# Kernel optimization log

Measured on AMD Instinct MI355X. Metric: run time of the kernel, lower is better.

Reference implementation:

```python
import jax, jax.numpy as jnp
import numpy as np
from jax import lax

T, H, I, E, K = 1024, 1024, 512, 16, 4


def setup_inputs() -> dict:
    key = jax.random.key(0)
    k1, k2, k3, k4, k5 = jax.random.split(key, 5)
    hidden_states = jax.random.normal(k1, (T, H), dtype=jnp.float32)
    top_k_index = jax.random.randint(k2, (T, K), 0, E)
    top_k_weights = jax.random.uniform(k3, (T, K), dtype=jnp.float32)
    gate_up_proj = jax.random.normal(k4, (E, 2 * I, H), dtype=jnp.float32) * 0.02
    down_proj = jax.random.normal(k5, (E, H, I), dtype=jnp.float32) * 0.02
    return {
        "hidden_states": hidden_states,
        "top_k_index": top_k_index,
        "top_k_weights": top_k_weights,
        "gate_up_proj": gate_up_proj,
        "down_proj": down_proj,
    }


def reference(hidden_states, top_k_index, top_k_weights, gate_up_proj, down_proj):
    num_experts = gate_up_proj.shape[0]
    # combine[t, e] = sum_k top_k_weights[t, k] * [top_k_index[t, k] == e]
    # Expert output is linear in the routing weight, so summing weights over
    # duplicate (token, expert) hits matches the original index_add_ exactly.
    one_hot = jax.nn.one_hot(top_k_index, num_experts, dtype=hidden_states.dtype)  # [T, K, E]
    combine = jnp.einsum("tke,tk->te", one_hot, top_k_weights)  # [T, E]

    def expert_step(acc, xs):
        w_gu, w_d, c = xs  # [2I, H], [H, I], [T]
        gu = hidden_states @ w_gu.T          # [T, 2I]
        gate, up = jnp.split(gu, 2, axis=-1)
        h = jax.nn.silu(gate) * up            # [T, I]
        out = h @ w_d.T                       # [T, H]
        return acc + out * c[:, None], None

    final, _ = lax.scan(
        expert_step,
        jnp.zeros_like(hidden_states),
        (gate_up_proj, down_proj, combine.T),
    )
    return final
```

## Files before the change

kernel.cpp:

```cpp
#include <hip/hip_runtime.h>
#include <hip/hip_bf16.h>
#include <cstdint>
#include <cstddef>

#define T_TOK 1024
#define HDIM  1024
#define IDIM  512
#define NEXP  16
#define TOPK  4
#define CAP   1024
#define GROUP 5

typedef __bf16 bf16;
typedef __attribute__((ext_vector_type(8))) __bf16 bf16x8;
typedef __attribute__((ext_vector_type(4))) __bf16 bf16x4;
typedef __attribute__((ext_vector_type(4))) float f32x4;

__device__ __forceinline__ void lds_load16(void* lds_dst, const void* g_src) {
  __builtin_amdgcn_global_load_lds(
      (__attribute__((address_space(1))) unsigned int*)(void*)(g_src),
      (__attribute__((address_space(3))) unsigned int*)(lds_dst),
      16, 0, 0);
}

__device__ __forceinline__ bf16x4 cvt4(float4 a) {
  bf16x4 o;
  o[0] = (bf16)a.x; o[1] = (bf16)a.y; o[2] = (bf16)a.z; o[3] = (bf16)a.w;
  return o;
}
__device__ __forceinline__ bf16x8 pack2(float4 a, float4 b) {
  bf16x8 o;
  o[0] = (bf16)a.x; o[1] = (bf16)a.y; o[2] = (bf16)a.z; o[3] = (bf16)a.w;
  o[4] = (bf16)b.x; o[5] = (bf16)b.y; o[6] = (bf16)b.z; o[7] = (bf16)b.w;
  return o;
}


#define CVT_BLOCKS (T_TOK * HDIM / 4 / 256)

__global__ void prep_kernel(const float* __restrict__ hid_f, bf16* __restrict__ hid_b,
                            const int* __restrict__ idx, const float* __restrict__ w,
                            int* __restrict__ etk, float* __restrict__ ew,
                            int* __restrict__ cntpad) {
  __shared__ int cnt;
  const int b = blockIdx.x;
  const int tid = threadIdx.x;
  if (b < CVT_BLOCKS) {
    int i = b * 256 + tid;
    float4 v = ((const float4*)hid_f)[i];
    ((bf16x4*)hid_b)[i] = cvt4(v);
    if (b == 0)
      ((bf16x4*)(hid_b + (size_t)T_TOK * HDIM))[tid] = cvt4(make_float4(0.f, 0.f, 0.f, 0.f));
    return;
  }
  const int e = b - CVT_BLOCKS;
  if (tid == 0) cnt = 0;
  __syncthreads();
  for (int j = tid; j < T_TOK * TOPK; j += blockDim.x) {
    if (idx[j] == e) {
      int slot = atomicAdd(&cnt, 1);
      if (slot < CAP) { etk[e * CAP + slot] = j; ew[e * CAP + slot] = w[j]; }
    }
  }
  __syncthreads();
  int c = cnt < CAP ? cnt : CAP;
  int p = (c + 63) & ~63;
  for (int j = c + tid; j < p; j += blockDim.x) {
    etk[e * CAP + j] = (T_TOK << 2);
    ew[e * CAP + j] = 0.f;
  }
  if (tid == 0) cntpad[e] = p;
}


__global__ __launch_bounds__(256, 2) void gemm1_kernel(
    const bf16* __restrict__ hid,
    const float* __restrict__ gup,
    const int* __restrict__ etk, const float* __restrict__ ew,
    const int* __restrict__ cntpad,
    bf16* __restrict__ hsc) {
  __shared__ __align__(16) bf16 As[GROUP][64 * 64];
  __shared__ __align__(16) bf16 BgS[16 * 64];
  __shared__ __align__(16) bf16 BuS[16 * 64];
  const int e  = blockIdx.y;
  const int trips = cntpad[e] >> 6;
  const int n0 = blockIdx.x * 16;
  const int ebase = e * CAP;
  const int tid = threadIdx.x, lane = tid & 63, wid = tid >> 6;
  const int wm = wid * 16;
  const int lcol = lane & 15, lquad = lane >> 4;
  const int srow = tid >> 3;
  const int swz  = ((tid & 7) ^ (srow & 7)) * 8;
  const int br = tid >> 4;
  const int bc = (tid & 15) * 4;
  const int wb = (((bc >> 3) ^ (br & 7)) * 8) + (bc & 7);
  const float* gBg = gup + (size_t)e * (2 * IDIM) * HDIM + (size_t)(n0 + br) * HDIM + bc;
  const float* gBu = gBg + (size_t)IDIM * HDIM;

  for (int mg = 0; mg < trips; mg += GROUP) {
    const int tg = trips - mg < GROUP ? trips - mg : GROUP;
    const bf16 *gA0[GROUP], *gA1[GROUP];
#pragma unroll
    for (int mt = 0; mt < GROUP; ++mt)
      if (mt < tg) {
        const int mb = ebase + (mg + mt) * 64;
        gA0[mt] = hid + (size_t)(etk[mb + srow] >> 2) * HDIM + swz;
        gA1[mt] = hid + (size_t)(etk[mb + srow + 32] >> 2) * HDIM + swz;
      }
    f32x4 aG[GROUP], aU[GROUP];
#pragma unroll
    for (int mt = 0; mt < GROUP; ++mt) {
      aG[mt] = f32x4{0.f, 0.f, 0.f, 0.f};
      aU[mt] = f32x4{0.f, 0.f, 0.f, 0.f};
    }
    for (int k = 0; k < HDIM / 64; ++k) {
      float4 vg = *(const float4*)(gBg + k * 64);
      float4 vu = *(const float4*)(gBu + k * 64);
      __syncthreads();
#pragma unroll
      for (int mt = 0; mt < GROUP; ++mt)
        if (mt < tg) {
          lds_load16(&As[mt][tid * 8],        gA0[mt] + k * 64);
          lds_load16(&As[mt][tid * 8 + 2048], gA1[mt] + k * 64);
        }
      *(bf16x4*)&BgS[br * 64 + wb] = cvt4(vg);
      *(bf16x4*)&BuS[br * 64 + wb] = cvt4(vu);
      __syncthreads();
#pragma unroll
      for (int ks = 0; ks < 2; ++ks) {
        const int lch = ks * 4 + lquad;
        bf16x8 bg = *(const bf16x8*)&BgS[lcol * 64 + ((lch ^ (lcol & 7)) * 8)];
        bf16x8 bu = *(const bf16x8*)&BuS[lcol * 64 + ((lch ^ (lcol & 7)) * 8)];
        const int ar = wm + lcol;
        const int aoff = ar * 64 + ((lch ^ (ar & 7)) * 8);
#pragma unroll
        for (int mt = 0; mt < GROUP; ++mt)
          if (mt < tg) {
            bf16x8 af = *(const bf16x8*)&As[mt][aoff];
            aG[mt] = __builtin_amdgcn_mfma_f32_16x16x32_bf16(af, bg, aG[mt], 0, 0, 0);
            aU[mt] = __builtin_amdgcn_mfma_f32_16x16x32_bf16(af, bu, aU[mt], 0, 0, 0);
          }
      }
    }
#pragma unroll
    for (int mt = 0; mt < GROUP; ++mt)
      if (mt < tg) {
#pragma unroll
        for (int rr = 0; rr < 4; ++rr) {
          const int erow = (mg + mt) * 64 + wm + lquad * 4 + rr;
          const float wgt = ew[ebase + erow];
          float g = aG[mt][rr], u = aU[mt][rr];
          float s = g / (1.f + __expf(-g));
          hsc[(size_t)(ebase + erow) * IDIM + n0 + lcol] = (bf16)(s * u * wgt);
        }
      }
  }
}


__global__ __launch_bounds__(256, 2) void gemm2_kernel(
    const bf16* __restrict__ hsc,
    const float* __restrict__ down,
    const int* __restrict__ etk, const int* __restrict__ cntpad,
    float* __restrict__ slabs) {
  __shared__ __align__(16) bf16 As[GROUP][64 * 64];
  __shared__ __align__(16) bf16 Bs[32 * 64];
  const int e  = blockIdx.y;
  const int trips = cntpad[e] >> 6;
  const int n0 = blockIdx.x * 32;
  const int ebase = e * CAP;
  const int tid = threadIdx.x, lane = tid & 63, wid = tid >> 6;
  const int wm = wid * 16;
  const int lcol = lane & 15, lquad = lane >> 4;
  const int srow = tid >> 3;
  const int swz  = ((tid & 7) ^ (srow & 7)) * 8;
  const int btr = tid >> 3;
  const int c0  = (tid & 7) * 8;
  const int wbk = ((tid & 7) ^ (btr & 7)) * 8;
  const float* gB = down + (size_t)e * HDIM * IDIM + (size_t)(n0 + btr) * IDIM + c0;

  for (int mg = 0; mg < trips; mg += GROUP) {
    const int tg = trips - mg < GROUP ? trips - mg : GROUP;
    f32x4 acc[GROUP][2];
#pragma unroll
    for (int mt = 0; mt < GROUP; ++mt) {
      acc[mt][0] = f32x4{0.f, 0.f, 0.f, 0.f};
      acc[mt][1] = f32x4{0.f, 0.f, 0.f, 0.f};
    }
    for (int k = 0; k < IDIM / 64; ++k) {
      float4 v0 = *(const float4*)(gB + k * 64);
      float4 v1 = *(const float4*)(gB + k * 64 + 4);
      __syncthreads();
#pragma unroll
      for (int mt = 0; mt < GROUP; ++mt)
        if (mt < tg) {
          const bf16* gA = hsc + (size_t)(ebase + (mg + mt) * 64 + srow) * IDIM + k * 64 + swz;
          lds_load16(&As[mt][tid * 8],        gA);
          lds_load16(&As[mt][tid * 8 + 2048], gA + (size_t)32 * IDIM);
        }
      *(bf16x8*)&Bs[btr * 64 + wbk] = pack2(v0, v1);
      __syncthreads();
#pragma unroll
      for (int ks = 0; ks < 2; ++ks) {
        const int lch = ks * 4 + lquad;
        const int br0 = lcol, br1 = 16 + lcol;
        bf16x8 b0 = *(const bf16x8*)&Bs[br0 * 64 + ((lch ^ (br0 & 7)) * 8)];
        bf16x8 b1 = *(const bf16x8*)&Bs[br1 * 64 + ((lch ^ (br1 & 7)) * 8)];
        const int ar = wm + lcol;
        const int aoff = ar * 64 + ((lch ^ (ar & 7)) * 8);
#pragma unroll
        for (int mt = 0; mt < GROUP; ++mt)
          if (mt < tg) {
            bf16x8 af = *(const bf16x8*)&As[mt][aoff];
            acc[mt][0] = __builtin_amdgcn_mfma_f32_16x16x32_bf16(af, b0, acc[mt][0], 0, 0, 0);
            acc[mt][1] = __builtin_amdgcn_mfma_f32_16x16x32_bf16(af, b1, acc[mt][1], 0, 0, 0);
          }
      }
    }
#pragma unroll
    for (int mt = 0; mt < GROUP; ++mt)
      if (mt < tg) {
#pragma unroll
        for (int rr = 0; rr < 4; ++rr) {
          const int tk = etk[ebase + (mg + mt) * 64 + wm + lquad * 4 + rr];
          const int tok = tk >> 2, kslot = tk & 3;
          float* orow = slabs + ((size_t)kslot * (T_TOK + 1) + tok) * HDIM + n0;
          orow[lcol]      = acc[mt][0][rr];
          orow[16 + lcol] = acc[mt][1][rr];
        }
      }
  }
}


__global__ void reduce_kernel(const float* __restrict__ slabs, float* __restrict__ out) {
  const size_t stride = (size_t)(T_TOK + 1) * HDIM;
  int i = blockIdx.x * blockDim.x + threadIdx.x;
  float4 a = ((const float4*)slabs)[i];
  float4 b = ((const float4*)(slabs + stride))[i];
  float4 c = ((const float4*)(slabs + 2 * stride))[i];
  float4 d = ((const float4*)(slabs + 3 * stride))[i];
  float4 o;
  o.x = a.x + b.x + c.x + d.x;
  o.y = a.y + b.y + c.y + d.y;
  o.z = a.z + b.z + c.z + d.z;
  o.w = a.w + b.w + c.w + d.w;
  ((float4*)out)[i] = o;
}


extern "C" void kernel_launch(void* const* d_in, const int* in_sizes, int n_in,
                              void* d_out, int out_size, void* d_ws, size_t ws_size,
                              hipStream_t stream) {
  const float* hid_f  = (const float*)d_in[0];
  const int*   idx    = (const int*)d_in[1];
  const float* tw     = (const float*)d_in[2];
  const float* gup_f  = (const float*)d_in[3];
  const float* down_f = (const float*)d_in[4];
  float* out = (float*)d_out;

  uint8_t* ws = (uint8_t*)d_ws;
  size_t off = 0;
  bf16* hid_b = (bf16*)(ws + off);   off += (size_t)(T_TOK + 1) * HDIM * 2;
  int*  etk   = (int*)(ws + off);    off += (size_t)NEXP * CAP * 4;
  float* ewt  = (float*)(ws + off);  off += (size_t)NEXP * CAP * 4;
  int* cntpad = (int*)(ws + off);    off += 256;
  bf16* hsc   = (bf16*)(ws + off);   off += (size_t)NEXP * CAP * IDIM * 2;
  float* slabs = (float*)(ws + off);

  prep_kernel<<<dim3(CVT_BLOCKS + NEXP), dim3(256), 0, stream>>>(
      hid_f, hid_b, idx, tw, etk, ewt, cntpad);
  gemm1_kernel<<<dim3(IDIM / 16, NEXP), dim3(256), 0, stream>>>(
      hid_b, gup_f, etk, ewt, cntpad, hsc);
  gemm2_kernel<<<dim3(HDIM / 32, NEXP), dim3(256), 0, stream>>>(
      hsc, down_f, etk, cntpad, slabs);
  reduce_kernel<<<dim3(T_TOK * HDIM / 4 / 256), dim3(256), 0, stream>>>(slabs, out);
}
```

Baseline: 191.9 us.

## Split M tiles across a z grid dimension and narrow gemm2 N tiles

Both expert GEMM kernels gain a second grid dimension that interleaves 64-row M tiles between two blocks, with GROUP cut from 5 to 3 and launch bounds raised to 4 blocks per CU. gemm2 also narrows its N tile from 32 to 16 columns, doubling its x-grid and using one accumulator per tile. The aim is more blocks and higher occupancy to fill the CUs on unbalanced per-expert workloads. In exchange, the fp32 weights are read and converted to bf16 twice as often per expert, and there is less A reuse per B tile.

```diff
diff --git a/kernel.cpp b/kernel.cpp
--- a/kernel.cpp
+++ b/kernel.cpp
@@ -9,7 +9,7 @@
 #define NEXP  16
 #define TOPK  4
 #define CAP   1024
-#define GROUP 5
+#define GROUP 3
 
 typedef __bf16 bf16;
 typedef __attribute__((ext_vector_type(8))) __bf16 bf16x8;
@@ -26,12 +26,6 @@
 __device__ __forceinline__ bf16x4 cvt4(float4 a) {
   bf16x4 o;
   o[0] = (bf16)a.x; o[1] = (bf16)a.y; o[2] = (bf16)a.z; o[3] = (bf16)a.w;
-  return o;
-}
-__device__ __forceinline__ bf16x8 pack2(float4 a, float4 b) {
-  bf16x8 o;
-  o[0] = (bf16)a.x; o[1] = (bf16)a.y; o[2] = (bf16)a.z; o[3] = (bf16)a.w;
-  o[4] = (bf16)b.x; o[5] = (bf16)b.y; o[6] = (bf16)b.z; o[7] = (bf16)b.w;
   return o;
 }
 
@@ -73,7 +67,7 @@
 }
 
 
-__global__ __launch_bounds__(256, 2) void gemm1_kernel(
+__global__ __launch_bounds__(256, 4) void gemm1_kernel(
     const bf16* __restrict__ hid,
     const float* __restrict__ gup,
     const int* __restrict__ etk, const float* __restrict__ ew,
@@ -83,6 +77,7 @@
   __shared__ __align__(16) bf16 BgS[16 * 64];
   __shared__ __align__(16) bf16 BuS[16 * 64];
   const int e  = blockIdx.y;
+  const int z  = blockIdx.z;
   const int trips = cntpad[e] >> 6;
   const int n0 = blockIdx.x * 16;
   const int ebase = e * CAP;
@@ -97,13 +92,14 @@
   const float* gBg = gup + (size_t)e * (2 * IDIM) * HDIM + (size_t)(n0 + br) * HDIM + bc;
   const float* gBu = gBg + (size_t)IDIM * HDIM;
 
-  for (int mg = 0; mg < trips; mg += GROUP) {
-    const int tg = trips - mg < GROUP ? trips - mg : GROUP;
+  for (int mg = z; mg < trips; mg += 2 * GROUP) {
+    int tg = (trips - mg + 1) >> 1;
+    if (tg > GROUP) tg = GROUP;
     const bf16 *gA0[GROUP], *gA1[GROUP];
 #pragma unroll
     for (int mt = 0; mt < GROUP; ++mt)
       if (mt < tg) {
-        const int mb = ebase + (mg + mt) * 64;
+        const int mb = ebase + (mg + 2 * mt) * 64;
         gA0[mt] = hid + (size_t)(etk[mb + srow] >> 2) * HDIM + swz;
         gA1[mt] = hid + (size_t)(etk[mb + srow + 32] >> 2) * HDIM + swz;
       }
@@ -147,7 +143,7 @@
       if (mt < tg) {
 #pragma unroll
         for (int rr = 0; rr < 4; ++rr) {
-          const int erow = (mg + mt) * 64 + wm + lquad * 4 + rr;
+          const int erow = (mg + 2 * mt) * 64 + wm + lquad * 4 + rr;
           const float wgt = ew[ebase + erow];
           float g = aG[mt][rr], u = aU[mt][rr];
           float s = g / (1.f + __expf(-g));
@@ -158,62 +154,65 @@
 }
 
 
-__global__ __launch_bounds__(256, 2) void gemm2_kernel(
+__global__ __launch_bounds__(256, 4) void gemm2_kernel(
     const bf16* __restrict__ hsc,
     const float* __restrict__ down,
     const int* __restrict__ etk, const int* __restrict__ cntpad,
     float* __restrict__ slabs) {
   __shared__ __align__(16) bf16 As[GROUP][64 * 64];
-  __shared__ __align__(16) bf16 Bs[32 * 64];
+  __shared__ __align__(16) bf16 Bs[16 * 64];
   const int e  = blockIdx.y;
+  const int z  = blockIdx.z;
   const int trips = cntpad[e] >> 6;
-  const int n0 = blockIdx.x * 32;
+  const int n0 = blockIdx.x * 16;
   const int ebase = e * CAP;
   const int tid = threadIdx.x, lane = tid & 63, wid = tid >> 6;
   const int wm = wid * 16;
   const int lcol = lane & 15, lquad = lane >> 4;
   const int srow = tid >> 3;
   const int swz  = ((tid & 7) ^ (srow & 7)) * 8;
-  const int btr = tid >> 3;
-  const int c0  = (tid & 7) * 8;
-  const int wbk = ((tid & 7) ^ (btr & 7)) * 8;
-  const float* gB = down + (size_t)e * HDIM * IDIM + (size_t)(n0 + btr) * IDIM + c0;
-
-  for (int mg = 0; mg < trips; mg += GROUP) {
-    const int tg = trips - mg < GROUP ? trips - mg : GROUP;
-    f32x4 acc[GROUP][2];
-#pragma unroll
-    for (int mt = 0; mt < GROUP; ++mt) {
-      acc[mt][0] = f32x4{0.f, 0.f, 0.f, 0.f};
-      acc[mt][1] = f32x4{0.f, 0.f, 0.f, 0.f};
-    }
+  const int br = tid >> 4;
+  const int bc = (tid & 15) * 4;
+  const int wb = (((bc >> 3) ^ (br & 7)) * 8) + (bc & 7);
+  const float* gB = down + (size_t)e * HDIM * IDIM + (size_t)(n0 + br) * IDIM + bc;
+
+  for (int mg = z; mg < trips; mg += 2 * GROUP) {
+    int tg = (trips - mg + 1) >> 1;
+    if (tg > GROUP) tg = GROUP;
+    const bf16 *gA0[GROUP], *gA1[GROUP];
+#pragma unroll
+    for (int mt = 0; mt < GROUP; ++mt)
+      if (mt < tg) {
+        const size_t rbase = (size_t)(ebase + (mg + 2 * mt) * 64);
+        gA0[mt] = hsc + (rbase + srow) * IDIM + swz;
+        gA1[mt] = hsc + (rbase + srow + 32) * IDIM + swz;
+      }
+    f32x4 acc[GROUP];
+#pragma unroll
+    for (int mt = 0; mt < GROUP; ++mt) acc[mt] = f32x4{0.f, 0.f, 0.f, 0.f};
+
     for (int k = 0; k < IDIM / 64; ++k) {
-      float4 v0 = *(const float4*)(gB + k * 64);
-      float4 v1 = *(const float4*)(gB + k * 64 + 4);
+      float4 vb = *(const float4*)(gB + k * 64);
       __syncthreads();
 #pragma unroll
       for (int mt = 0; mt < GROUP; ++mt)
         if (mt < tg) {
-          const bf16* gA = hsc + (size_t)(ebase + (mg + mt) * 64 + srow) * IDIM + k * 64 + swz;
-          lds_load16(&As[mt][tid * 8],        gA);
-          lds_load16(&As[mt][tid * 8 + 2048], gA + (size_t)32 * IDIM);
-        }
-      *(bf16x8*)&Bs[btr * 64 + wbk] = pack2(v0, v1);
+          lds_load16(&As[mt][tid * 8],        gA0[mt] + k * 64);
+          lds_load16(&As[mt][tid * 8 + 2048], gA1[mt] + k * 64);
+        }
+      *(bf16x4*)&Bs[br * 64 + wb] = cvt4(vb);
       __syncthreads();
 #pragma unroll
       for (int ks = 0; ks < 2; ++ks) {
         const int lch = ks * 4 + lquad;
-        const int br0 = lcol, br1 = 16 + lcol;
-        bf16x8 b0 = *(const bf16x8*)&Bs[br0 * 64 + ((lch ^ (br0 & 7)) * 8)];
-        bf16x8 b1 = *(const bf16x8*)&Bs[br1 * 64 + ((lch ^ (br1 & 7)) * 8)];
+        bf16x8 bv = *(const bf16x8*)&Bs[lcol * 64 + ((lch ^ (lcol & 7)) * 8)];
         const int ar = wm + lcol;
         const int aoff = ar * 64 + ((lch ^ (ar & 7)) * 8);
 #pragma unroll
         for (int mt = 0; mt < GROUP; ++mt)
           if (mt < tg) {
             bf16x8 af = *(const bf16x8*)&As[mt][aoff];
-            acc[mt][0] = __builtin_amdgcn_mfma_f32_16x16x32_bf16(af, b0, acc[mt][0], 0, 0, 0);
-            acc[mt][1] = __builtin_amdgcn_mfma_f32_16x16x32_bf16(af, b1, acc[mt][1], 0, 0, 0);
+            acc[mt] = __builtin_amdgcn_mfma_f32_16x16x32_bf16(af, bv, acc[mt], 0, 0, 0);
           }
       }
     }
@@ -222,11 +221,9 @@
       if (mt < tg) {
 #pragma unroll
         for (int rr = 0; rr < 4; ++rr) {
-          const int tk = etk[ebase + (mg + mt) * 64 + wm + lquad * 4 + rr];
+          const int tk = etk[ebase + (mg + 2 * mt) * 64 + wm + lquad * 4 + rr];
           const int tok = tk >> 2, kslot = tk & 3;
-          float* orow = slabs + ((size_t)kslot * (T_TOK + 1) + tok) * HDIM + n0;
-          orow[lcol]      = acc[mt][0][rr];
-          orow[16 + lcol] = acc[mt][1][rr];
+          slabs[((size_t)kslot * (T_TOK + 1) + tok) * HDIM + n0 + lcol] = acc[mt][rr];
         }
       }
   }
@@ -270,9 +267,9 @@
 
   prep_kernel<<<dim3(CVT_BLOCKS + NEXP), dim3(256), 0, stream>>>(
       hid_f, hid_b, idx, tw, etk, ewt, cntpad);
-  gemm1_kernel<<<dim3(IDIM / 16, NEXP), dim3(256), 0, stream>>>(
+  gemm1_kernel<<<dim3(IDIM / 16, NEXP, 2), dim3(256), 0, stream>>>(
       hid_b, gup_f, etk, ewt, cntpad, hsc);
-  gemm2_kernel<<<dim3(HDIM / 32, NEXP), dim3(256), 0, stream>>>(
+  gemm2_kernel<<<dim3(HDIM / 16, NEXP, 2), dim3(256), 0, stream>>>(
       hsc, down_f, etk, cntpad, slabs);
   reduce_kernel<<<dim3(T_TOK * HDIM / 4 / 256), dim3(256), 0, stream>>>(slabs, out);
 }
```

Measured after the change: 190.8 us. No clear change (-0.5%).
